# Optimization experiments

Hardware: AMD Instinct MI355X
Metric: run time of the kernel (lower is better)

Reference implementation:

```python
import jax, jax.numpy as jnp
import numpy as np

B, TX, TY, D, H = 8, 128, 128, 512, 512
LN_EPS = 1e-3  # keras LayerNormalization default epsilon


def setup_inputs() -> dict:
    key = jax.random.key(0)
    ks = jax.random.split(key, 6)
    scale = 1.0 / np.sqrt(D)
    return {
        "context": jax.random.normal(ks[0], (B, TX, D), jnp.float32),
        "x": jax.random.normal(ks[1], (B, TY, D), jnp.float32),
        "Wa": jax.random.normal(ks[2], (D, H), jnp.float32) * scale,
        "bWa": jnp.zeros((H,), jnp.float32),
        "Ua": jax.random.normal(ks[3], (D, H), jnp.float32) * scale,
        "bUa": jnp.zeros((H,), jnp.float32),
        "Va": jax.random.normal(ks[4], (H, 1), jnp.float32) * (1.0 / np.sqrt(H)),
        "bVa": jnp.zeros((1,), jnp.float32),
        "gamma": jnp.ones((D,), jnp.float32),
        "beta": jnp.zeros((D,), jnp.float32),
    }


def reference(context, x, Wa, bWa, Ua, bUa, Va, bVa, gamma, beta):
    # context: [B,Tx,D], x: [B,Ty,D]
    Wc = context @ Wa + bWa                      # [B,Tx,H]
    Ux = x @ Ua + bUa                            # [B,Ty,H]
    t = jnp.tanh(Wc[:, None, :, :] + Ux[:, :, None, :])  # [B,Ty,Tx,H]
    scores = jnp.einsum('btxh,h->btx', t, Va[:, 0]) + bVa[0]  # [B,Ty,Tx]
    attn = jax.nn.softmax(scores, axis=-1)
    cv = jnp.einsum('btx,bxd->btd', attn, context)  # [B,Ty,D]
    mean = jnp.mean(cv, axis=-1, keepdims=True)
    var = jnp.mean(jnp.square(cv - mean), axis=-1, keepdims=True)
    cv = (cv - mean) * jax.lax.rsqrt(var + LN_EPS) * gamma + beta
    return cv + x
```

## Files before the change

### kernel.cpp

```cpp
#include <hip/hip_runtime.h>


#define SCALE 2.8853900817779268f

typedef __attribute__((ext_vector_type(8))) short short8;
typedef float floatx4 __attribute__((ext_vector_type(4)));

__device__ __forceinline__ unsigned pack_bf_trunc(float lo, float hi) {
  return __builtin_amdgcn_perm(__float_as_uint(hi), __float_as_uint(lo),
                               0x07060302u);
}

__global__ __launch_bounds__(512) void gemm_all(
    const float* __restrict__ ctx, const float* __restrict__ xin,
    const float* __restrict__ Wa, const float* __restrict__ Ua,
    const float* __restrict__ bWa, const float* __restrict__ bUa,
    float* __restrict__ WcT, float* __restrict__ Ux) {
  const bool second = (blockIdx.z != 0);
  const float* __restrict__ A = second ? xin : ctx;
  const float* __restrict__ W = second ? Ua : Wa;
  const int m0 = blockIdx.x * 32, n0 = blockIdx.y * 64;

  __shared__ __align__(16) unsigned short As[512 * 8];
  __shared__ __align__(16) unsigned short Bs[1024 * 8];

  const int t = threadIdx.x;
  const int lane = t & 63, wv = t >> 6;

  const int arow = ((t >> 6) & 1) * 16 + (t & 15);
  const int ak   = (t >> 7) * 32 + ((t & 63) >> 4) * 8;
  const float* aptr = A + (size_t)(m0 + arow) * 512 + ak;

  const int bn0_ = ((t >> 6) & 3) * 16 + (t & 15);
  const int bk0_ = (t >> 8) * 32 + ((t & 63) >> 4) * 8;
  const int s2 = t + 512;
  const int bn1_ = ((s2 >> 6) & 3) * 16 + (s2 & 15);
  const int bk1_ = (s2 >> 8) * 32 + ((s2 & 63) >> 4) * 8;
  const float* bptr0 = W + (size_t)bk0_ * 512 + n0 + bn0_;
  const float* bptr1 = W + (size_t)bk1_ * 512 + n0 + bn1_;

  const int wm = wv & 1, wn = wv >> 1;
  floatx4 acc = {};

  float4 a0 = *(const float4*)(aptr);
  float4 a1 = *(const float4*)(aptr + 4);
  float bw0[8], bw1[8];
#pragma unroll
  for (int j = 0; j < 8; j++) {
    bw0[j] = bptr0[(size_t)j * 512];
    bw1[j] = bptr1[(size_t)j * 512];
  }

  for (int kt = 0; kt < 512; kt += 128) {
    union { short8 s; uint4 u; } av, bv0, bv1;
    av.u.x = pack_bf_trunc(a0.x, a0.y);
    av.u.y = pack_bf_trunc(a0.z, a0.w);
    av.u.z = pack_bf_trunc(a1.x, a1.y);
    av.u.w = pack_bf_trunc(a1.z, a1.w);
    bv0.u.x = pack_bf_trunc(bw0[0], bw0[1]);
    bv0.u.y = pack_bf_trunc(bw0[2], bw0[3]);
    bv0.u.z = pack_bf_trunc(bw0[4], bw0[5]);
    bv0.u.w = pack_bf_trunc(bw0[6], bw0[7]);
    bv1.u.x = pack_bf_trunc(bw1[0], bw1[1]);
    bv1.u.y = pack_bf_trunc(bw1[2], bw1[3]);
    bv1.u.z = pack_bf_trunc(bw1[4], bw1[5]);
    bv1.u.w = pack_bf_trunc(bw1[6], bw1[7]);
    ((short8*)As)[t] = av.s;
    ((short8*)Bs)[t] = bv0.s;
    ((short8*)Bs)[t + 512] = bv1.s;
    __syncthreads();
    if (kt + 128 < 512) {
      a0 = *(const float4*)(aptr + kt + 128);
      a1 = *(const float4*)(aptr + kt + 132);
      const float* p0 = bptr0 + (size_t)(kt + 128) * 512;
      const float* p1 = bptr1 + (size_t)(kt + 128) * 512;
#pragma unroll
      for (int j = 0; j < 8; j++) {
        bw0[j] = p0[(size_t)j * 512];
        bw1[j] = p1[(size_t)j * 512];
      }
    }
#pragma unroll
    for (int ks = 0; ks < 4; ks++) {
      const short8 af = ((const short8*)As)[ks * 128 + wm * 64 + lane];
      const short8 bf = ((const short8*)Bs)[ks * 256 + wn * 64 + lane];
      acc = __builtin_amdgcn_mfma_f32_16x16x32_bf16(af, bf, acc, 0, 0, 0);
    }
    __syncthreads();
  }

  const int quad = lane >> 4;
  const int h = n0 + wn * 16 + (lane & 15);
  const int mg0 = m0 + wm * 16 + quad * 4;
  if (!second) {
    const float bias = bWa[h] + bUa[h];
    const int b = mg0 >> 7, tx0 = mg0 & 127;
    float4 o;
    o.x = (acc[0] + bias) * SCALE;
    o.y = (acc[1] + bias) * SCALE;
    o.z = (acc[2] + bias) * SCALE;
    o.w = (acc[3] + bias) * SCALE;
    *(float4*)&WcT[(size_t)b * 65536 + (size_t)h * 128 + tx0] = o;
  } else {
#pragma unroll
    for (int r = 0; r < 4; r++)
      Ux[(size_t)(mg0 + r) * 512 + h] = acc[r] * SCALE;
  }
}

__global__ __launch_bounds__(1024) void attn4(
    const float* __restrict__ WcT, const float* __restrict__ Ux,
    const float* __restrict__ ctx, const float* __restrict__ xin,
    const float* __restrict__ Va,
    const float* __restrict__ gamma, const float* __restrict__ beta,
    float* __restrict__ out) {
  const int b = blockIdx.x >> 5;
  const int ty0 = (blockIdx.x & 31) * 4;
  const int t = threadIdx.x;
  const int lane = t & 63, wv = t >> 6;

  __shared__ __align__(16) float4 s_ux[512];
  __shared__ float s_va[512];
  __shared__ float s_part[32][128];
  __shared__ __align__(16) float4 s_at[128];
  __shared__ float s_red[4][2][8];
  __shared__ float s_mv[4][2];

  {
    const float* uxb = Ux + (size_t)(b * 128 + ty0) * 512;
    for (int i = t; i < 2048; i += 1024) {
      const int r = i >> 9, h = i & 511;
      ((float*)&s_ux[h])[r] = uxb[i];
    }
    if (t < 512) s_va[t] = Va[t];
  }
  __syncthreads();

  const int tx = t & 127, hq = t >> 7;
  {
    const float* wp = WcT + (size_t)b * 65536 + (size_t)hq * 8192 + tx;
    float a0 = 0.f, a1 = 0.f, a2 = 0.f, a3 = 0.f;
#pragma unroll 4
    for (int hh = 0; hh < 64; hh++) {
      const float w = wp[(size_t)hh * 128];
      const float4 u = s_ux[hq * 64 + hh];
      const float va = s_va[hq * 64 + hh];
      a0 = fmaf(va, __builtin_amdgcn_rcpf(1.0f + __builtin_amdgcn_exp2f(w + u.x)), a0);
      a1 = fmaf(va, __builtin_amdgcn_rcpf(1.0f + __builtin_amdgcn_exp2f(w + u.y)), a1);
      a2 = fmaf(va, __builtin_amdgcn_rcpf(1.0f + __builtin_amdgcn_exp2f(w + u.z)), a2);
      a3 = fmaf(va, __builtin_amdgcn_rcpf(1.0f + __builtin_amdgcn_exp2f(w + u.w)), a3);
    }
    s_part[hq * 4 + 0][tx] = a0;
    s_part[hq * 4 + 1][tx] = a1;
    s_part[hq * 4 + 2][tx] = a2;
    s_part[hq * 4 + 3][tx] = a3;
  }
  __syncthreads();

  if (wv < 4) {
    const int r = wv;
    float sA = 0.f, sB = 0.f;
#pragma unroll
    for (int q = 0; q < 8; q++) {
      sA += s_part[q * 4 + r][lane];
      sB += s_part[q * 4 + r][lane + 64];
    }
    sA *= -2.0f; sB *= -2.0f;
    float m = fmaxf(sA, sB);
#pragma unroll
    for (int off = 32; off; off >>= 1) m = fmaxf(m, __shfl_xor(m, off));
    const float eA = __expf(sA - m);
    const float eB = __expf(sB - m);
    float sm = eA + eB;
#pragma unroll
    for (int off = 32; off; off >>= 1) sm += __shfl_xor(sm, off);
    const float inv = __builtin_amdgcn_rcpf(sm);
    ((float*)&s_at[lane])[r] = eA * inv;
    ((float*)&s_at[lane + 64])[r] = eB * inv;
  }
  __syncthreads();

  const int d = t & 511, rh = t >> 9;
  float cv0 = 0.f, cv1 = 0.f;
  {
    const float* cp = ctx + (size_t)b * 65536 + d;
#pragma unroll 4
    for (int x = 0; x < 128; x++) {
      const float c = cp[(size_t)x * 512];
      const float2 at = *(const float2*)((const float*)&s_at[x] + rh * 2);
      cv0 = fmaf(at.x, c, cv0);
      cv1 = fmaf(at.y, c, cv1);
    }
  }

  const int wh = wv & 7;
#pragma unroll
  for (int j = 0; j < 2; j++) {
    const float v = j ? cv1 : cv0;
    float sm = v, q = v * v;
#pragma unroll
    for (int off = 32; off; off >>= 1) {
      sm += __shfl_xor(sm, off);
      q += __shfl_xor(q, off);
    }
    if (lane == 0) {
      s_red[rh * 2 + j][0][wh] = sm;
      s_red[rh * 2 + j][1][wh] = q;
    }
  }
  __syncthreads();
  if (t < 4) {
    float sm = 0.f, q = 0.f;
#pragma unroll
    for (int i = 0; i < 8; i++) { sm += s_red[t][0][i]; q += s_red[t][1][i]; }
    const float mean = sm * (1.0f / 512.0f);
    const float var = q * (1.0f / 512.0f) - mean * mean;
    s_mv[t][0] = mean;
    s_mv[t][1] = __builtin_amdgcn_rsqf(var + 1e-3f);
  }
  __syncthreads();

  {
    const float g = gamma[d], bb = beta[d];
#pragma unroll
    for (int j = 0; j < 2; j++) {
      const int r = rh * 2 + j;
      const int row = b * 128 + ty0 + r;
      const float v = j ? cv1 : cv0;
      const float xv = xin[(size_t)row * 512 + d];
      out[(size_t)row * 512 + d] = (v - s_mv[r][0]) * s_mv[r][1] * g + bb + xv;
    }
  }
}

extern "C" void kernel_launch(void* const* d_in, const int* in_sizes, int n_in,
                              void* d_out, int out_size, void* d_ws, size_t ws_size,
                              hipStream_t stream) {
  const float* ctx   = (const float*)d_in[0];
  const float* xin   = (const float*)d_in[1];
  const float* Wa    = (const float*)d_in[2];
  const float* bWa   = (const float*)d_in[3];
  const float* Ua    = (const float*)d_in[4];
  const float* bUa   = (const float*)d_in[5];
  const float* Va    = (const float*)d_in[6];
  const float* gamma = (const float*)d_in[8];
  const float* beta  = (const float*)d_in[9];
  float* out = (float*)d_out;

  char* ws = (char*)d_ws;
  float* WcT = (float*)ws;
  float* Ux  = (float*)(ws + (2u << 20));

  gemm_all<<<dim3(32, 8, 2), 512, 0, stream>>>(ctx, xin, Wa, Ua, bWa, bUa, WcT, Ux);
  attn4<<<256, 1024, 0, stream>>>(WcT, Ux, ctx, xin, Va, gamma, beta, out);
}
```

Before: 109.3 us.

## Split attention kernel into 512 blocks of two query rows with swizzled ordering

The attention kernel now handles two query rows per block with 512 threads, launching 512 blocks instead of 256 blocks of 1024 threads that each handle four rows. Block indices are swizzled so neighbouring blocks map to different batches. The first eight context rows, gamma, beta and the residual x are prefetched before the softmax barrier to hide load latency. The aim is more blocks across the 256 CUs and lower tail latency, at the cost of each block reloading WcT and context with half the reuse per load.

```diff
diff --git a/kernel.cpp b/kernel.cpp
--- a/kernel.cpp
+++ b/kernel.cpp
@@ -108,62 +108,72 @@
   }
 }
 
-__global__ __launch_bounds__(1024) void attn4(
+__global__ __launch_bounds__(512) void attn2(
     const float* __restrict__ WcT, const float* __restrict__ Ux,
     const float* __restrict__ ctx, const float* __restrict__ xin,
     const float* __restrict__ Va,
     const float* __restrict__ gamma, const float* __restrict__ beta,
     float* __restrict__ out) {
-  const int b = blockIdx.x >> 5;
-  const int ty0 = (blockIdx.x & 31) * 4;
+  const int lb = ((blockIdx.x & 7) << 6) | (blockIdx.x >> 3);
+  const int b = lb >> 6;
+  const int ty0 = (lb & 63) * 2;
   const int t = threadIdx.x;
   const int lane = t & 63, wv = t >> 6;
 
-  __shared__ __align__(16) float4 s_ux[512];
+  __shared__ __align__(8) float2 s_ux[512];
   __shared__ float s_va[512];
-  __shared__ float s_part[32][128];
-  __shared__ __align__(16) float4 s_at[128];
-  __shared__ float s_red[4][2][8];
-  __shared__ float s_mv[4][2];
+  __shared__ float s_part[8][128];
+  __shared__ __align__(8) float2 s_at[128];
+  __shared__ float s_red[2][2][8];
+  __shared__ float s_mv[2][2];
 
   {
     const float* uxb = Ux + (size_t)(b * 128 + ty0) * 512;
-    for (int i = t; i < 2048; i += 1024) {
-      const int r = i >> 9, h = i & 511;
-      ((float*)&s_ux[h])[r] = uxb[i];
-    }
-    if (t < 512) s_va[t] = Va[t];
+#pragma unroll
+    for (int i = 0; i < 2; i++) {
+      const int idx = t + i * 512;
+      ((float*)&s_ux[idx & 511])[idx >> 9] = uxb[idx];
+    }
+    s_va[t] = Va[t];
   }
   __syncthreads();
 
   const int tx = t & 127, hq = t >> 7;
   {
-    const float* wp = WcT + (size_t)b * 65536 + (size_t)hq * 8192 + tx;
-    float a0 = 0.f, a1 = 0.f, a2 = 0.f, a3 = 0.f;
+    const float* wp = WcT + (size_t)b * 65536 + (size_t)hq * 16384 + tx;
+    const float2* up = &s_ux[hq * 128];
+    const float* vap = &s_va[hq * 128];
+    float a0 = 0.f, a1 = 0.f;
 #pragma unroll 4
-    for (int hh = 0; hh < 64; hh++) {
+    for (int hh = 0; hh < 128; hh++) {
       const float w = wp[(size_t)hh * 128];
-      const float4 u = s_ux[hq * 64 + hh];
-      const float va = s_va[hq * 64 + hh];
+      const float2 u = up[hh];
+      const float va = vap[hh];
       a0 = fmaf(va, __builtin_amdgcn_rcpf(1.0f + __builtin_amdgcn_exp2f(w + u.x)), a0);
       a1 = fmaf(va, __builtin_amdgcn_rcpf(1.0f + __builtin_amdgcn_exp2f(w + u.y)), a1);
-      a2 = fmaf(va, __builtin_amdgcn_rcpf(1.0f + __builtin_amdgcn_exp2f(w + u.z)), a2);
-      a3 = fmaf(va, __builtin_amdgcn_rcpf(1.0f + __builtin_amdgcn_exp2f(w + u.w)), a3);
-    }
-    s_part[hq * 4 + 0][tx] = a0;
-    s_part[hq * 4 + 1][tx] = a1;
-    s_part[hq * 4 + 2][tx] = a2;
-    s_part[hq * 4 + 3][tx] = a3;
-  }
-  __syncthreads();
-
-  if (wv < 4) {
+    }
+    s_part[hq * 2 + 0][tx] = a0;
+    s_part[hq * 2 + 1][tx] = a1;
+  }
+  __syncthreads();
+
+  const int d = t;
+  const float* cp = ctx + (size_t)b * 65536 + d;
+  float cpre[8];
+#pragma unroll
+  for (int k = 0; k < 8; k++) cpre[k] = cp[(size_t)k * 512];
+  const float g = gamma[d], bb = beta[d];
+  const int row0 = b * 128 + ty0;
+  const float xv0 = xin[(size_t)row0 * 512 + d];
+  const float xv1 = xin[(size_t)(row0 + 1) * 512 + d];
+
+  if (wv < 2) {
     const int r = wv;
     float sA = 0.f, sB = 0.f;
 #pragma unroll
-    for (int q = 0; q < 8; q++) {
-      sA += s_part[q * 4 + r][lane];
-      sB += s_part[q * 4 + r][lane + 64];
+    for (int q = 0; q < 4; q++) {
+      sA += s_part[q * 2 + r][lane];
+      sB += s_part[q * 2 + r][lane + 64];
     }
     sA *= -2.0f; sB *= -2.0f;
     float m = fmaxf(sA, sB);
@@ -180,36 +190,35 @@
   }
   __syncthreads();
 
-  const int d = t & 511, rh = t >> 9;
   float cv0 = 0.f, cv1 = 0.f;
+#pragma unroll
+  for (int k = 0; k < 8; k++) {
+    const float2 at = s_at[k];
+    cv0 = fmaf(at.x, cpre[k], cv0);
+    cv1 = fmaf(at.y, cpre[k], cv1);
+  }
+#pragma unroll 4
+  for (int x = 8; x < 128; x++) {
+    const float c = cp[(size_t)x * 512];
+    const float2 at = s_at[x];
+    cv0 = fmaf(at.x, c, cv0);
+    cv1 = fmaf(at.y, c, cv1);
+  }
+
   {
-    const float* cp = ctx + (size_t)b * 65536 + d;
-#pragma unroll 4
-    for (int x = 0; x < 128; x++) {
-      const float c = cp[(size_t)x * 512];
-      const float2 at = *(const float2*)((const float*)&s_at[x] + rh * 2);
-      cv0 = fmaf(at.x, c, cv0);
-      cv1 = fmaf(at.y, c, cv1);
-    }
-  }
-
-  const int wh = wv & 7;
-#pragma unroll
-  for (int j = 0; j < 2; j++) {
-    const float v = j ? cv1 : cv0;
-    float sm = v, q = v * v;
+    float sm0 = cv0, q0 = cv0 * cv0, sm1 = cv1, q1 = cv1 * cv1;
 #pragma unroll
     for (int off = 32; off; off >>= 1) {
-      sm += __shfl_xor(sm, off);
-      q += __shfl_xor(q, off);
+      sm0 += __shfl_xor(sm0, off); q0 += __shfl_xor(q0, off);
+      sm1 += __shfl_xor(sm1, off); q1 += __shfl_xor(q1, off);
     }
     if (lane == 0) {
-      s_red[rh * 2 + j][0][wh] = sm;
-      s_red[rh * 2 + j][1][wh] = q;
-    }
-  }
-  __syncthreads();
-  if (t < 4) {
+      s_red[0][0][wv] = sm0; s_red[0][1][wv] = q0;
+      s_red[1][0][wv] = sm1; s_red[1][1][wv] = q1;
+    }
+  }
+  __syncthreads();
+  if (t < 2) {
     float sm = 0.f, q = 0.f;
 #pragma unroll
     for (int i = 0; i < 8; i++) { sm += s_red[t][0][i]; q += s_red[t][1][i]; }
@@ -220,17 +229,8 @@
   }
   __syncthreads();
 
-  {
-    const float g = gamma[d], bb = beta[d];
-#pragma unroll
-    for (int j = 0; j < 2; j++) {
-      const int r = rh * 2 + j;
-      const int row = b * 128 + ty0 + r;
-      const float v = j ? cv1 : cv0;
-      const float xv = xin[(size_t)row * 512 + d];
-      out[(size_t)row * 512 + d] = (v - s_mv[r][0]) * s_mv[r][1] * g + bb + xv;
-    }
-  }
+  out[(size_t)row0 * 512 + d]       = (cv0 - s_mv[0][0]) * s_mv[0][1] * g + bb + xv0;
+  out[(size_t)(row0 + 1) * 512 + d] = (cv1 - s_mv[1][0]) * s_mv[1][1] * g + bb + xv1;
 }
 
 extern "C" void kernel_launch(void* const* d_in, const int* in_sizes, int n_in,
@@ -252,5 +252,5 @@
   float* Ux  = (float*)(ws + (2u << 20));
 
   gemm_all<<<dim3(32, 8, 2), 512, 0, stream>>>(ctx, xin, Wa, Ua, bWa, bUa, WcT, Ux);
-  attn4<<<256, 1024, 0, stream>>>(WcT, Ux, ctx, xin, Va, gamma, beta, out);
-}
+  attn2<<<512, 512, 0, stream>>>(WcT, Ux, ctx, xin, Va, gamma, beta, out);
+}
```

New measurement: 110.0 us. About the same (+0.6%).
